# Kernel optimization log

Measured on AMD Instinct MI355X. Metric: run time of the kernel, lower is better.

The kernel has to match this reference:

```python
import jax, jax.numpy as jnp
import numpy as np

N = 100000
E = 1600000
F_IN = 602
NHID = 128
N_CLS = 41


def setup_inputs() -> dict:
    key = jax.random.key(0)
    k1, k2, k3, k4 = jax.random.split(key, 4)
    x = jax.random.normal(k1, (N, F_IN), dtype=jnp.float32)
    edge_index = jax.random.randint(k2, (2, E), 0, N, dtype=jnp.int64)
    # Glorot-style scaled weights
    W1 = jax.random.normal(k3, (F_IN, NHID), dtype=jnp.float32) * (1.0 / np.sqrt(F_IN))
    b1 = jnp.zeros((NHID,), dtype=jnp.float32)
    W2 = jax.random.normal(k4, (NHID, N_CLS), dtype=jnp.float32) * (1.0 / np.sqrt(NHID))
    b2 = jnp.zeros((N_CLS,), dtype=jnp.float32)
    return {"x": x, "edge_index": edge_index, "W1": W1, "b1": b1, "W2": W2, "b2": b2}


def reference(x, edge_index, W1, b1, W2, b2):
    n = x.shape[0]
    loop = jnp.arange(n, dtype=edge_index.dtype)
    # PyG GCNConv: add self-loops, symmetric normalization D^-1/2 (A+I) D^-1/2
    src = jnp.concatenate([edge_index[0], loop])  # [E+N]
    dst = jnp.concatenate([edge_index[1], loop])  # [E+N]
    ones = jnp.ones(src.shape[0], dtype=x.dtype)
    deg = jax.ops.segment_sum(ones, dst, num_segments=n)  # in-degree incl self-loop
    dinv = jnp.where(deg > 0, jax.lax.rsqrt(deg), 0.0)
    norm = dinv[src] * dinv[dst]  # [E+N]

    def conv(h, W, b):
        h = h @ W  # transform first (smaller feature dim for gather)
        msg = h[src] * norm[:, None]  # gather + scale
        return jax.ops.segment_sum(msg, dst, num_segments=n) + b  # scatter-add

    h = jax.nn.relu(conv(x, W1, b1))
    # dropout is identity in eval mode
    out = conv(h, W2, b2)
    return jax.nn.log_softmax(out, axis=1)
```

## Files before the change

### kernel.cpp

```cpp
#include <hip/hip_runtime.h>
#include <math.h>

#define GK 602
#define GH 128
#define GC 41
#define GCP 48
#define KPAD 608
#define GS 40

typedef __bf16 bf16x8 __attribute__((ext_vector_type(8)));
typedef __bf16 bf16x4 __attribute__((ext_vector_type(4)));
typedef float f32x16 __attribute__((ext_vector_type(16)));

__device__ __forceinline__ unsigned short f2bf(float f) {
    __bf16 b = (__bf16)f;
    return __builtin_bit_cast(unsigned short, b);
}
__device__ __forceinline__ float bf2f(unsigned short u) {
    return __uint_as_float((unsigned int)u << 16);
}
__device__ __forceinline__ float bflo(unsigned int u) { return __uint_as_float(u << 16); }
__device__ __forceinline__ float bfhi(unsigned int u) { return __uint_as_float(u & 0xffff0000u); }


__global__ void k_hist(const int* __restrict__ dst, int* __restrict__ counts, int E) {
    int e = blockIdx.x * 256 + threadIdx.x;
    if (e < E) atomicAdd(&counts[dst[e]], 1);
}

__global__ void k_scan_a(const int* __restrict__ counts, int* __restrict__ row_ptr,
                         int* __restrict__ bsum, int n) {
    __shared__ int svals[256];
    __shared__ int soffs[256];
    int t = threadIdx.x;
    int base = blockIdx.x * 1024 + t * 4;
    int v[4];
    int s = 0;
#pragma unroll
    for (int j = 0; j < 4; ++j) {
        int idx = base + j;
        v[j] = (idx < n) ? counts[idx] : 0;
        s += v[j];
    }
    svals[t] = s;
    __syncthreads();
    if (t == 0) {
        int acc = 0;
        for (int i = 0; i < 256; ++i) { int tmp = svals[i]; soffs[i] = acc; acc += tmp; }
        bsum[blockIdx.x] = acc;
    }
    __syncthreads();
    int off = soffs[t];
#pragma unroll
    for (int j = 0; j < 4; ++j) {
        int idx = base + j;
        if (idx < n) row_ptr[idx] = off;
        off += v[j];
    }
}

__global__ void k_scan_b(int* __restrict__ bsum, int nb) {
    if (threadIdx.x == 0 && blockIdx.x == 0) {
        int acc = 0;
        for (int i = 0; i < nb; ++i) { int t = bsum[i]; bsum[i] = acc; acc += t; }
    }
}

__global__ void k_scan_c(int* __restrict__ row_ptr, const int* __restrict__ bsum, int n, int E) {
    int i = blockIdx.x * 256 + threadIdx.x;
    if (i < n) row_ptr[i] += bsum[i >> 10];
    if (i == 0) row_ptr[n] = E;
}

__global__ void k_dinv_cursor(const int* __restrict__ counts, const int* __restrict__ row_ptr,
                              float* __restrict__ dinv, int* __restrict__ cursor, int n) {
    int i = blockIdx.x * 256 + threadIdx.x;
    if (i < n) {
        dinv[i] = rsqrtf((float)(counts[i] + 1));
        cursor[i] = row_ptr[i];
    }
}

__global__ void k_fill(const int* __restrict__ src, const int* __restrict__ dst,
                       const float* __restrict__ dinv,
                       int* __restrict__ cursor, int2* __restrict__ meta, int E) {
    int e = blockIdx.x * 256 + threadIdx.x;
    if (e < E) {
        int s = src[e];
        int d = dst[e];
        int p = atomicAdd(&cursor[d], 1);
        float w = dinv[s] * dinv[d];
        meta[p] = make_int2(s, __float_as_int(w));
    }
}


__global__ void k_prepW1(const float* __restrict__ W1, unsigned short* __restrict__ W1T) {
    int i = blockIdx.x * 256 + threadIdx.x;
    if (i >= GH * KPAD) return;
    int n = i / KPAD;
    int k = i - n * KPAD;
    float v = (k < GK) ? W1[(size_t)k * GH + n] : 0.f;
    W1T[i] = f2bf(v);
}


__global__ __launch_bounds__(256) void k_gemm1_mfma(const float* __restrict__ X,
                                                    const unsigned short* __restrict__ W1T,
                                                    unsigned short* __restrict__ Y, int M) {
    __shared__ __bf16 As[128 * GS];
    __shared__ __bf16 Bs[128 * GS];
    int tid = threadIdx.x;
    int lane = tid & 63;
    int w = tid >> 6;
    int row0 = blockIdx.x * 128;

    f32x16 acc[4];
#pragma unroll
    for (int c = 0; c < 4; ++c)
#pragma unroll
        for (int i = 0; i < 16; ++i) acc[c][i] = 0.f;

    int sr = tid >> 3;
    int sk = (tid & 7) * 4;
    int am = 32 * w + (lane & 31);
    int kh = (lane >> 5) * 8;
    int bn = lane & 31;

    for (int k0 = 0; k0 < KPAD; k0 += 32) {
#pragma unroll
        for (int p = 0; p < 4; ++p) {
            int r = sr + 32 * p;
            int gr = row0 + r;
            int gk = k0 + sk;
            float4 v = make_float4(0.f, 0.f, 0.f, 0.f);
            if (gr < M) {
                if (gk + 4 <= GK) {
                    v = *(const float4*)&X[(size_t)gr * GK + gk];
                } else {
                    float t0 = (gk + 0 < GK) ? X[(size_t)gr * GK + gk + 0] : 0.f;
                    float t1 = (gk + 1 < GK) ? X[(size_t)gr * GK + gk + 1] : 0.f;
                    float t2 = (gk + 2 < GK) ? X[(size_t)gr * GK + gk + 2] : 0.f;
                    float t3 = (gk + 3 < GK) ? X[(size_t)gr * GK + gk + 3] : 0.f;
                    v = make_float4(t0, t1, t2, t3);
                }
            }
            bf16x4 b4;
            b4[0] = (__bf16)v.x; b4[1] = (__bf16)v.y; b4[2] = (__bf16)v.z; b4[3] = (__bf16)v.w;
            *(bf16x4*)&As[r * GS + sk] = b4;
        }
#pragma unroll
        for (int s = 0; s < 2; ++s) {
            int slot = tid + 256 * s;
            int n = slot >> 2;
            int j = slot & 3;
            uint4 v = *(const uint4*)&W1T[(size_t)n * KPAD + k0 + 8 * j];
            *(uint4*)&Bs[n * GS + 8 * j] = v;
        }
        __syncthreads();
#pragma unroll
        for (int t = 0; t < 2; ++t) {
            bf16x8 af = *(const bf16x8*)&As[am * GS + 16 * t + kh];
#pragma unroll
            for (int c = 0; c < 4; ++c) {
                bf16x8 bf = *(const bf16x8*)&Bs[(32 * c + bn) * GS + 16 * t + kh];
                acc[c] = __builtin_amdgcn_mfma_f32_32x32x16_bf16(af, bf, acc[c], 0, 0, 0);
            }
        }
        __syncthreads();
    }
#pragma unroll
    for (int c = 0; c < 4; ++c) {
#pragma unroll
        for (int reg = 0; reg < 16; ++reg) {
            int rrow = (reg & 3) + 8 * (reg >> 2) + 4 * (lane >> 5);
            int grow = row0 + 32 * w + rrow;
            int gcol = 32 * c + (lane & 31);
            if (grow < M) Y[(size_t)grow * GH + gcol] = f2bf(acc[c][reg]);
        }
    }
}


__global__ __launch_bounds__(256) void k_agg1(const unsigned int* __restrict__ H,
                                              unsigned int* __restrict__ O,
                                              const int* __restrict__ row_ptr,
                                              const int2* __restrict__ meta,
                                              const float* __restrict__ dinv,
                                              const float* __restrict__ bias, int n) {
    int wv = threadIdx.x >> 6;
    int lane = threadIdx.x & 63;
    int d = blockIdx.x * 4 + wv;
    if (d >= n) return;
    float dd = dinv[d];
    int beg = row_ptr[d], end = row_ptr[d + 1];
    unsigned int v = H[(size_t)d * 64 + lane];
    float sw = dd * dd;
    float a0 = sw * bflo(v);
    float a1 = sw * bfhi(v);
    int e = beg;
    for (; e + 4 <= end; e += 4) {
        int2 m0 = meta[e + 0];
        int2 m1 = meta[e + 1];
        int2 m2 = meta[e + 2];
        int2 m3 = meta[e + 3];
        unsigned int u0 = H[(size_t)m0.x * 64 + lane];
        unsigned int u1 = H[(size_t)m1.x * 64 + lane];
        unsigned int u2 = H[(size_t)m2.x * 64 + lane];
        unsigned int u3 = H[(size_t)m3.x * 64 + lane];
        float w0 = __int_as_float(m0.y);
        float w1 = __int_as_float(m1.y);
        float w2 = __int_as_float(m2.y);
        float w3 = __int_as_float(m3.y);
        a0 = fmaf(w0, bflo(u0), a0); a1 = fmaf(w0, bfhi(u0), a1);
        a0 = fmaf(w1, bflo(u1), a0); a1 = fmaf(w1, bfhi(u1), a1);
        a0 = fmaf(w2, bflo(u2), a0); a1 = fmaf(w2, bfhi(u2), a1);
        a0 = fmaf(w3, bflo(u3), a0); a1 = fmaf(w3, bfhi(u3), a1);
    }
    for (; e < end; ++e) {
        int2 m = meta[e];
        unsigned int u = H[(size_t)m.x * 64 + lane];
        float w = __int_as_float(m.y);
        a0 = fmaf(w, bflo(u), a0);
        a1 = fmaf(w, bfhi(u), a1);
    }
    a0 = fmaxf(a0 + bias[2 * lane], 0.f);
    a1 = fmaxf(a1 + bias[2 * lane + 1], 0.f);
    O[(size_t)d * 64 + lane] = (unsigned int)f2bf(a0) | ((unsigned int)f2bf(a1) << 16);
}


__global__ __launch_bounds__(256) void k_gemm2t(const unsigned int* __restrict__ Hb,
                                                const float* __restrict__ W2,
                                                unsigned short* __restrict__ G, int n) {
    __shared__ float ws[128][GCP];
    for (int i = threadIdx.x; i < 128 * GCP; i += 256) {
        int k = i / GCP;
        int c = i - k * GCP;
        ws[k][c] = (c < GC) ? W2[k * GC + c] : 0.f;
    }
    __syncthreads();
    int r0 = blockIdx.x * 512 + threadIdx.x;
    int r1 = r0 + 256;
    bool v0 = r0 < n, v1 = r1 < n;
    float acc0[GCP], acc1[GCP];
#pragma unroll
    for (int c = 0; c < GCP; ++c) { acc0[c] = 0.f; acc1[c] = 0.f; }
    const uint2* h0 = (const uint2*)(Hb + (size_t)(v0 ? r0 : 0) * 64);
    const uint2* h1 = (const uint2*)(Hb + (size_t)(v1 ? r1 : 0) * 64);
    for (int q = 0; q < 32; ++q) {
        uint2 ua = h0[q];
        uint2 ub = h1[q];
        float va[4] = {bflo(ua.x), bfhi(ua.x), bflo(ua.y), bfhi(ua.y)};
        float vb[4] = {bflo(ub.x), bfhi(ub.x), bflo(ub.y), bfhi(ub.y)};
#pragma unroll
        for (int j = 0; j < 4; ++j) {
            int k = 4 * q + j;
#pragma unroll
            for (int cq = 0; cq < GCP / 4; ++cq) {
                float4 wv = *(const float4*)&ws[k][4 * cq];
                acc0[4 * cq + 0] = fmaf(va[j], wv.x, acc0[4 * cq + 0]);
                acc0[4 * cq + 1] = fmaf(va[j], wv.y, acc0[4 * cq + 1]);
                acc0[4 * cq + 2] = fmaf(va[j], wv.z, acc0[4 * cq + 2]);
                acc0[4 * cq + 3] = fmaf(va[j], wv.w, acc0[4 * cq + 3]);
                acc1[4 * cq + 0] = fmaf(vb[j], wv.x, acc1[4 * cq + 0]);
                acc1[4 * cq + 1] = fmaf(vb[j], wv.y, acc1[4 * cq + 1]);
                acc1[4 * cq + 2] = fmaf(vb[j], wv.z, acc1[4 * cq + 2]);
                acc1[4 * cq + 3] = fmaf(vb[j], wv.w, acc1[4 * cq + 3]);
            }
        }
    }
    if (v0) {
#pragma unroll
        for (int c = 0; c < GCP; ++c) G[(size_t)r0 * GCP + c] = f2bf(acc0[c]);
    }
    if (v1) {
#pragma unroll
        for (int c = 0; c < GCP; ++c) G[(size_t)r1 * GCP + c] = f2bf(acc1[c]);
    }
}


__global__ __launch_bounds__(256) void k_agg2(const unsigned short* __restrict__ G,
                                              float* __restrict__ out,
                                              const int* __restrict__ row_ptr,
                                              const int2* __restrict__ meta,
                                              const float* __restrict__ dinv,
                                              const float* __restrict__ b2, int n) {
    int wv = threadIdx.x >> 6;
    int lane = threadIdx.x & 63;
    int gl = (lane < GCP) ? lane : (GCP - 1);
    int d = blockIdx.x * 4 + wv;
    if (d >= n) return;
    float dd = dinv[d];
    int beg = row_ptr[d], end = row_ptr[d + 1];
    float a = dd * dd * bf2f(G[(size_t)d * GCP + gl]);
    int e = beg;
    for (; e + 4 <= end; e += 4) {
        int2 m0 = meta[e + 0];
        int2 m1 = meta[e + 1];
        int2 m2 = meta[e + 2];
        int2 m3 = meta[e + 3];
        unsigned short u0 = G[(size_t)m0.x * GCP + gl];
        unsigned short u1 = G[(size_t)m1.x * GCP + gl];
        unsigned short u2 = G[(size_t)m2.x * GCP + gl];
        unsigned short u3 = G[(size_t)m3.x * GCP + gl];
        a = fmaf(__int_as_float(m0.y), bf2f(u0), a);
        a = fmaf(__int_as_float(m1.y), bf2f(u1), a);
        a = fmaf(__int_as_float(m2.y), bf2f(u2), a);
        a = fmaf(__int_as_float(m3.y), bf2f(u3), a);
    }
    for (; e < end; ++e) {
        int2 m = meta[e];
        unsigned short u = G[(size_t)m.x * GCP + gl];
        a = fmaf(__int_as_float(m.y), bf2f(u), a);
    }
    float logit = (lane < GC) ? (a + b2[lane]) : -INFINITY;
    float mx = logit;
#pragma unroll
    for (int off = 32; off; off >>= 1) mx = fmaxf(mx, __shfl_xor(mx, off));
    float ex = (lane < GC) ? __expf(logit - mx) : 0.f;
    float sm = ex;
#pragma unroll
    for (int off = 32; off; off >>= 1) sm += __shfl_xor(sm, off);
    if (lane < GC) out[(size_t)d * GC + lane] = logit - mx - __logf(sm);
}


static inline size_t alignup256(size_t x) { return (x + 255) & ~(size_t)255; }

extern "C" void kernel_launch(void* const* d_in, const int* in_sizes, int n_in,
                              void* d_out, int out_size, void* d_ws, size_t ws_size,
                              hipStream_t stream) {
    const float* x  = (const float*)d_in[0];
    const int*   ei = (const int*)d_in[1];
    const float* W1 = (const float*)d_in[2];
    const float* b1 = (const float*)d_in[3];
    const float* W2 = (const float*)d_in[4];
    const float* b2 = (const float*)d_in[5];
    float* out = (float*)d_out;

    const int n = in_sizes[0] / GK;
    const int E = in_sizes[1] / 2;
    const int* src = ei;
    const int* dst = ei + E;

    char* w = (char*)d_ws;
    char* p;
    p = w; w += alignup256((size_t)n * 4);            float* dinv  = (float*)p;
    p = w; w += alignup256((size_t)n * 4);            int* counts  = (int*)p;
    p = w; w += alignup256((size_t)n * 4);            int* cursor  = (int*)p;
    p = w; w += alignup256((size_t)(n + 1) * 4);      int* row_ptr = (int*)p;
    p = w; w += alignup256(1024 * 4);                 int* bsum    = (int*)p;
    p = w; w += alignup256((size_t)E * 8);            int2* meta   = (int2*)p;
    p = w; w += alignup256((size_t)GH * KPAD * 2);    unsigned short* W1T = (unsigned short*)p;
    p = w; w += alignup256((size_t)n * GH * 2);       unsigned short* bufA = (unsigned short*)p;
    p = w; w += alignup256((size_t)n * GH * 2);       unsigned short* bufB = (unsigned short*)p;
    p = w; w += alignup256((size_t)n * GCP * 2);      unsigned short* G    = (unsigned short*)p;

    hipMemsetAsync(counts, 0, (size_t)n * 4, stream);

    int gE = (E + 255) / 256;
    int gN = (n + 255) / 256;
    int nb = (n + 1023) / 1024;

    k_hist<<<gE, 256, 0, stream>>>(dst, counts, E);
    k_scan_a<<<nb, 256, 0, stream>>>(counts, row_ptr, bsum, n);
    k_scan_b<<<1, 64, 0, stream>>>(bsum, nb);
    k_scan_c<<<gN, 256, 0, stream>>>(row_ptr, bsum, n, E);
    k_dinv_cursor<<<gN, 256, 0, stream>>>(counts, row_ptr, dinv, cursor, n);
    k_fill<<<gE, 256, 0, stream>>>(src, dst, dinv, cursor, meta, E);

    k_prepW1<<<(GH * KPAD + 255) / 256, 256, 0, stream>>>(W1, W1T);
    k_gemm1_mfma<<<(n + 127) / 128, 256, 0, stream>>>(x, W1T, bufA, n);
    k_agg1<<<(n + 3) / 4, 256, 0, stream>>>((const unsigned int*)bufA, (unsigned int*)bufB,
                                            row_ptr, meta, dinv, b1, n);
    k_gemm2t<<<(n + 511) / 512, 256, 0, stream>>>((const unsigned int*)bufB, W2, G, n);
    k_agg2<<<(n + 3) / 4, 256, 0, stream>>>(G, out, row_ptr, meta, dinv, b2, n);
}
```

Baseline: 729.7 us.

## Double-buffer GEMM1 B tiles, load A directly to registers, parallelize scans, fuse dinv

The first GEMM now reads X straight into registers in the MFMA fragment layout, with no A staging in shared memory. It double-buffers the W1 tile in LDS and prefetches the next A fragment, so global loads overlap with MFMAs and each iteration needs one barrier instead of two. The CSR scans use wave shuffles and a parallel block scan instead of serial single-thread loops, and the dinv/cursor kernel is merged into the scan fixup, removing one launch. Both aggregation kernels unroll the edge loop to 8 to keep more gathers in flight, at the cost of more registers.

```diff
diff --git a/kernel.cpp b/kernel.cpp
--- a/kernel.cpp
+++ b/kernel.cpp
@@ -30,9 +30,10 @@
 
 __global__ void k_scan_a(const int* __restrict__ counts, int* __restrict__ row_ptr,
                          int* __restrict__ bsum, int n) {
-    __shared__ int svals[256];
-    __shared__ int soffs[256];
+    __shared__ int wsum[4];
     int t = threadIdx.x;
+    int lane = t & 63;
+    int wv = t >> 6;
     int base = blockIdx.x * 1024 + t * 4;
     int v[4];
     int s = 0;
@@ -42,15 +43,19 @@
         v[j] = (idx < n) ? counts[idx] : 0;
         s += v[j];
     }
-    svals[t] = s;
+    int incl = s;
+#pragma unroll
+    for (int o = 1; o < 64; o <<= 1) {
+        int x = __shfl_up(incl, o);
+        if (lane >= o) incl += x;
+    }
+    if (lane == 63) wsum[wv] = incl;
     __syncthreads();
-    if (t == 0) {
-        int acc = 0;
-        for (int i = 0; i < 256; ++i) { int tmp = svals[i]; soffs[i] = acc; acc += tmp; }
-        bsum[blockIdx.x] = acc;
-    }
-    __syncthreads();
-    int off = soffs[t];
+    int woff = 0;
+#pragma unroll
+    for (int i = 0; i < 3; ++i) woff += (i < wv) ? wsum[i] : 0;
+    if (t == 255) bsum[blockIdx.x] = woff + incl;
+    int off = woff + incl - s;
 #pragma unroll
     for (int j = 0; j < 4; ++j) {
         int idx = base + j;
@@ -60,25 +65,31 @@
 }
 
 __global__ void k_scan_b(int* __restrict__ bsum, int nb) {
-    if (threadIdx.x == 0 && blockIdx.x == 0) {
-        int acc = 0;
-        for (int i = 0; i < nb; ++i) { int t = bsum[i]; bsum[i] = acc; acc += t; }
-    }
-}
-
-__global__ void k_scan_c(int* __restrict__ row_ptr, const int* __restrict__ bsum, int n, int E) {
-    int i = blockIdx.x * 256 + threadIdx.x;
-    if (i < n) row_ptr[i] += bsum[i >> 10];
-    if (i == 0) row_ptr[n] = E;
-}
-
-__global__ void k_dinv_cursor(const int* __restrict__ counts, const int* __restrict__ row_ptr,
-                              float* __restrict__ dinv, int* __restrict__ cursor, int n) {
+    __shared__ int sh[256];
+    int t = threadIdx.x;
+    int v = (t < nb) ? bsum[t] : 0;
+    sh[t] = v;
+    __syncthreads();
+    for (int o = 1; o < 256; o <<= 1) {
+        int x = (t >= o) ? sh[t - o] : 0;
+        __syncthreads();
+        sh[t] += x;
+        __syncthreads();
+    }
+    if (t < nb) bsum[t] = sh[t] - v;
+}
+
+__global__ void k_scan_c(int* __restrict__ row_ptr, const int* __restrict__ bsum,
+                         const int* __restrict__ counts, float* __restrict__ dinv,
+                         int* __restrict__ cursor, int n, int E) {
     int i = blockIdx.x * 256 + threadIdx.x;
     if (i < n) {
+        int rp = row_ptr[i] + bsum[i >> 10];
+        row_ptr[i] = rp;
+        cursor[i] = rp;
         dinv[i] = rsqrtf((float)(counts[i] + 1));
-        cursor[i] = row_ptr[i];
-    }
+    }
+    if (i == 0) row_ptr[n] = E;
 }
 
 __global__ void k_fill(const int* __restrict__ src, const int* __restrict__ dst,
@@ -105,69 +116,98 @@
 }
 
 
+struct AF { float4 v0, v1, v2, v3; };
+
+__device__ __forceinline__ AF loadA(const float* __restrict__ xr, int kb, bool tail) {
+    AF r;
+    if (!tail) {
+        r.v0 = *(const float4*)(xr + kb);
+        r.v1 = *(const float4*)(xr + kb + 4);
+        r.v2 = *(const float4*)(xr + kb + 16);
+        r.v3 = *(const float4*)(xr + kb + 20);
+    } else {
+        float tv[8], tw[8];
+#pragma unroll
+        for (int j = 0; j < 8; ++j) {
+            int k0_ = kb + j;
+            int k1_ = kb + 16 + j;
+            tv[j] = (k0_ < GK) ? xr[k0_] : 0.f;
+            tw[j] = (k1_ < GK) ? xr[k1_] : 0.f;
+        }
+        r.v0 = make_float4(tv[0], tv[1], tv[2], tv[3]);
+        r.v1 = make_float4(tv[4], tv[5], tv[6], tv[7]);
+        r.v2 = make_float4(tw[0], tw[1], tw[2], tw[3]);
+        r.v3 = make_float4(tw[4], tw[5], tw[6], tw[7]);
+    }
+    return r;
+}
+
+__device__ __forceinline__ bf16x8 cvt8(float4 a, float4 b) {
+    bf16x8 r;
+    r[0] = (__bf16)a.x; r[1] = (__bf16)a.y; r[2] = (__bf16)a.z; r[3] = (__bf16)a.w;
+    r[4] = (__bf16)b.x; r[5] = (__bf16)b.y; r[6] = (__bf16)b.z; r[7] = (__bf16)b.w;
+    return r;
+}
+
+__device__ __forceinline__ void stageB(const unsigned short* __restrict__ W1T,
+                                       __bf16* __restrict__ Bsb, int tid, int k0) {
+#pragma unroll
+    for (int s = 0; s < 2; ++s) {
+        int slot = tid + 256 * s;
+        int n = slot >> 2;
+        int j = slot & 3;
+        uint4 v = *(const uint4*)&W1T[(size_t)n * KPAD + k0 + 8 * j];
+        *(uint4*)&Bsb[n * GS + 8 * j] = v;
+    }
+}
+
 __global__ __launch_bounds__(256) void k_gemm1_mfma(const float* __restrict__ X,
                                                     const unsigned short* __restrict__ W1T,
                                                     unsigned short* __restrict__ Y, int M) {
-    __shared__ __bf16 As[128 * GS];
-    __shared__ __bf16 Bs[128 * GS];
+    __shared__ __bf16 Bs[2][128 * GS];
     int tid = threadIdx.x;
     int lane = tid & 63;
     int w = tid >> 6;
     int row0 = blockIdx.x * 128;
-
-    f32x16 acc[4];
-#pragma unroll
-    for (int c = 0; c < 4; ++c)
-#pragma unroll
-        for (int i = 0; i < 16; ++i) acc[c][i] = 0.f;
-
-    int sr = tid >> 3;
-    int sk = (tid & 7) * 4;
-    int am = 32 * w + (lane & 31);
+    int amr = 32 * w + (lane & 31);
+    int grow_base = row0 + amr;
+    int arow = (grow_base < M) ? grow_base : (M - 1);
+    const float* xr = X + (size_t)arow * GK;
     int kh = (lane >> 5) * 8;
     int bn = lane & 31;
 
-    for (int k0 = 0; k0 < KPAD; k0 += 32) {
-#pragma unroll
-        for (int p = 0; p < 4; ++p) {
-            int r = sr + 32 * p;
-            int gr = row0 + r;
-            int gk = k0 + sk;
-            float4 v = make_float4(0.f, 0.f, 0.f, 0.f);
-            if (gr < M) {
-                if (gk + 4 <= GK) {
-                    v = *(const float4*)&X[(size_t)gr * GK + gk];
-                } else {
-                    float t0 = (gk + 0 < GK) ? X[(size_t)gr * GK + gk + 0] : 0.f;
-                    float t1 = (gk + 1 < GK) ? X[(size_t)gr * GK + gk + 1] : 0.f;
-                    float t2 = (gk + 2 < GK) ? X[(size_t)gr * GK + gk + 2] : 0.f;
-                    float t3 = (gk + 3 < GK) ? X[(size_t)gr * GK + gk + 3] : 0.f;
-                    v = make_float4(t0, t1, t2, t3);
-                }
-            }
-            bf16x4 b4;
-            b4[0] = (__bf16)v.x; b4[1] = (__bf16)v.y; b4[2] = (__bf16)v.z; b4[3] = (__bf16)v.w;
-            *(bf16x4*)&As[r * GS + sk] = b4;
-        }
-#pragma unroll
-        for (int s = 0; s < 2; ++s) {
-            int slot = tid + 256 * s;
-            int n = slot >> 2;
-            int j = slot & 3;
-            uint4 v = *(const uint4*)&W1T[(size_t)n * KPAD + k0 + 8 * j];
-            *(uint4*)&Bs[n * GS + 8 * j] = v;
+    f32x16 acc[4];
+#pragma unroll
+    for (int c = 0; c < 4; ++c)
+#pragma unroll
+        for (int i = 0; i < 16; ++i) acc[c][i] = 0.f;
+
+    stageB(W1T, Bs[0], tid, 0);
+    AF a = loadA(xr, kh, false);
+    __syncthreads();
+
+    int buf = 0;
+    for (int it = 0; it < 19; ++it) {
+        AF an;
+        if (it < 18) {
+            stageB(W1T, Bs[buf ^ 1], tid, 32 * (it + 1));
+            an = loadA(xr, kh + 32 * (it + 1), it == 17);
+        }
+        bf16x8 af0 = cvt8(a.v0, a.v1);
+        bf16x8 af1 = cvt8(a.v2, a.v3);
+#pragma unroll
+        for (int c = 0; c < 4; ++c) {
+            bf16x8 b0 = *(const bf16x8*)&Bs[buf][(32 * c + bn) * GS + kh];
+            acc[c] = __builtin_amdgcn_mfma_f32_32x32x16_bf16(af0, b0, acc[c], 0, 0, 0);
+        }
+#pragma unroll
+        for (int c = 0; c < 4; ++c) {
+            bf16x8 b1 = *(const bf16x8*)&Bs[buf][(32 * c + bn) * GS + 16 + kh];
+            acc[c] = __builtin_amdgcn_mfma_f32_32x32x16_bf16(af1, b1, acc[c], 0, 0, 0);
         }
         __syncthreads();
-#pragma unroll
-        for (int t = 0; t < 2; ++t) {
-            bf16x8 af = *(const bf16x8*)&As[am * GS + 16 * t + kh];
-#pragma unroll
-            for (int c = 0; c < 4; ++c) {
-                bf16x8 bf = *(const bf16x8*)&Bs[(32 * c + bn) * GS + 16 * t + kh];
-                acc[c] = __builtin_amdgcn_mfma_f32_32x32x16_bf16(af, bf, acc[c], 0, 0, 0);
-            }
-        }
-        __syncthreads();
+        buf ^= 1;
+        a = an;
     }
 #pragma unroll
     for (int c = 0; c < 4; ++c) {
@@ -199,30 +239,41 @@
     float a0 = sw * bflo(v);
     float a1 = sw * bfhi(v);
     int e = beg;
-    for (; e + 4 <= end; e += 4) {
-        int2 m0 = meta[e + 0];
-        int2 m1 = meta[e + 1];
-        int2 m2 = meta[e + 2];
-        int2 m3 = meta[e + 3];
-        unsigned int u0 = H[(size_t)m0.x * 64 + lane];
-        unsigned int u1 = H[(size_t)m1.x * 64 + lane];
-        unsigned int u2 = H[(size_t)m2.x * 64 + lane];
-        unsigned int u3 = H[(size_t)m3.x * 64 + lane];
-        float w0 = __int_as_float(m0.y);
-        float w1 = __int_as_float(m1.y);
-        float w2 = __int_as_float(m2.y);
-        float w3 = __int_as_float(m3.y);
-        a0 = fmaf(w0, bflo(u0), a0); a1 = fmaf(w0, bfhi(u0), a1);
-        a0 = fmaf(w1, bflo(u1), a0); a1 = fmaf(w1, bfhi(u1), a1);
-        a0 = fmaf(w2, bflo(u2), a0); a1 = fmaf(w2, bfhi(u2), a1);
-        a0 = fmaf(w3, bflo(u3), a0); a1 = fmaf(w3, bfhi(u3), a1);
+    for (; e + 8 <= end; e += 8) {
+        int2 m[8];
+        unsigned int u[8];
+#pragma unroll
+        for (int j = 0; j < 8; ++j) m[j] = meta[e + j];
+#pragma unroll
+        for (int j = 0; j < 8; ++j) u[j] = H[(size_t)m[j].x * 64 + lane];
+#pragma unroll
+        for (int j = 0; j < 8; ++j) {
+            float wj = __int_as_float(m[j].y);
+            a0 = fmaf(wj, bflo(u[j]), a0);
+            a1 = fmaf(wj, bfhi(u[j]), a1);
+        }
+    }
+    if (e + 4 <= end) {
+        int2 m[4];
+        unsigned int u[4];
+#pragma unroll
+        for (int j = 0; j < 4; ++j) m[j] = meta[e + j];
+#pragma unroll
+        for (int j = 0; j < 4; ++j) u[j] = H[(size_t)m[j].x * 64 + lane];
+#pragma unroll
+        for (int j = 0; j < 4; ++j) {
+            float wj = __int_as_float(m[j].y);
+            a0 = fmaf(wj, bflo(u[j]), a0);
+            a1 = fmaf(wj, bfhi(u[j]), a1);
+        }
+        e += 4;
     }
     for (; e < end; ++e) {
         int2 m = meta[e];
         unsigned int u = H[(size_t)m.x * 64 + lane];
-        float w = __int_as_float(m.y);
-        a0 = fmaf(w, bflo(u), a0);
-        a1 = fmaf(w, bfhi(u), a1);
+        float wj = __int_as_float(m.y);
+        a0 = fmaf(wj, bflo(u), a0);
+        a1 = fmaf(wj, bfhi(u), a1);
     }
     a0 = fmaxf(a0 + bias[2 * lane], 0.f);
     a1 = fmaxf(a1 + bias[2 * lane + 1], 0.f);
@@ -296,24 +347,30 @@
     int beg = row_ptr[d], end = row_ptr[d + 1];
     float a = dd * dd * bf2f(G[(size_t)d * GCP + gl]);
     int e = beg;
-    for (; e + 4 <= end; e += 4) {
-        int2 m0 = meta[e + 0];
-        int2 m1 = meta[e + 1];
-        int2 m2 = meta[e + 2];
-        int2 m3 = meta[e + 3];
-        unsigned short u0 = G[(size_t)m0.x * GCP + gl];
-        unsigned short u1 = G[(size_t)m1.x * GCP + gl];
-        unsigned short u2 = G[(size_t)m2.x * GCP + gl];
-        unsigned short u3 = G[(size_t)m3.x * GCP + gl];
-        a = fmaf(__int_as_float(m0.y), bf2f(u0), a);
-        a = fmaf(__int_as_float(m1.y), bf2f(u1), a);
-        a = fmaf(__int_as_float(m2.y), bf2f(u2), a);
-        a = fmaf(__int_as_float(m3.y), bf2f(u3), a);
+    for (; e + 8 <= end; e += 8) {
+        int2 m[8];
+        unsigned short u[8];
+#pragma unroll
+        for (int j = 0; j < 8; ++j) m[j] = meta[e + j];
+#pragma unroll
+        for (int j = 0; j < 8; ++j) u[j] = G[(size_t)m[j].x * GCP + gl];
+#pragma unroll
+        for (int j = 0; j < 8; ++j) a = fmaf(__int_as_float(m[j].y), bf2f(u[j]), a);
+    }
+    if (e + 4 <= end) {
+        int2 m[4];
+        unsigned short u[4];
+#pragma unroll
+        for (int j = 0; j < 4; ++j) m[j] = meta[e + j];
+#pragma unroll
+        for (int j = 0; j < 4; ++j) u[j] = G[(size_t)m[j].x * GCP + gl];
+#pragma unroll
+        for (int j = 0; j < 4; ++j) a = fmaf(__int_as_float(m[j].y), bf2f(u[j]), a);
+        e += 4;
     }
     for (; e < end; ++e) {
         int2 m = meta[e];
-        unsigned short u = G[(size_t)m.x * GCP + gl];
-        a = fmaf(__int_as_float(m.y), bf2f(u), a);
+        a = fmaf(__int_as_float(m.y), bf2f(G[(size_t)m.x * GCP + gl]), a);
     }
     float logit = (lane < GC) ? (a + b2[lane]) : -INFINITY;
     float mx = logit;
@@ -366,9 +423,8 @@
 
     k_hist<<<gE, 256, 0, stream>>>(dst, counts, E);
     k_scan_a<<<nb, 256, 0, stream>>>(counts, row_ptr, bsum, n);
-    k_scan_b<<<1, 64, 0, stream>>>(bsum, nb);
-    k_scan_c<<<gN, 256, 0, stream>>>(row_ptr, bsum, n, E);
-    k_dinv_cursor<<<gN, 256, 0, stream>>>(counts, row_ptr, dinv, cursor, n);
+    k_scan_b<<<1, 256, 0, stream>>>(bsum, nb);
+    k_scan_c<<<gN, 256, 0, stream>>>(row_ptr, bsum, counts, dinv, cursor, n, E);
     k_fill<<<gE, 256, 0, stream>>>(src, dst, dinv, cursor, meta, E);
 
     k_prepW1<<<(GH * KPAD + 255) / 256, 256, 0, stream>>>(W1, W1T);
```

After: 726.7 us. About the same (-0.4%).
